# Kernel optimization log

Measured on AMD Instinct MI355X. Metric: run time of the kernel, lower is better.

## Reference

```python
import jax, jax.numpy as jnp
import numpy as np

K = 32
BN_EPS = 1e-5


def _fps(points, n_samples):
    # Sequential farthest point sampling; deterministic start at index 0
    # (torch version uses a random start; math otherwise identical).
    B, N, _ = points.shape

    def step(carry, _):
        dist_min, far = carry                                   # (B,N), (B,)
        c = jnp.take_along_axis(points, far[:, None, None].astype(jnp.int32) * jnp.ones((1, 1, 3), jnp.int32), axis=1)  # (B,1,3)
        d = jnp.sum((points - c) ** 2, axis=2)                  # (B,N)
        dist_min = jnp.minimum(dist_min, d)
        return (dist_min, jnp.argmax(dist_min, axis=1)), far

    init = (jnp.full((B, N), 1e10, points.dtype), jnp.zeros((B,), jnp.int64).astype(jnp.int32))
    _, cent = jax.lax.scan(step, init, None, length=n_samples)  # (n_samples, B)
    return cent.T                                               # (B, n_samples)


def _knn_idx(cntrds, pnts, k):
    # squared euclidean distance (same neighbor ordering as torch.cdist)
    d2 = (jnp.sum(cntrds ** 2, -1)[:, :, None]
          + jnp.sum(pnts ** 2, -1)[:, None, :]
          - 2.0 * jnp.einsum('bsc,bnc->bsn', cntrds, pnts))     # (B,ns,N)
    _, idx = jax.lax.top_k(-d2, k)                              # smallest-k
    return idx                                                  # (B,ns,k)


def _gather(x, idx):
    # x: (B,N,D), idx: (B,...) -> (B,...,D)
    return jax.vmap(lambda a, i: a[i])(x, idx)


def _conv1x1(x, w):
    # x: (B,Cin,ns,k), w: (Cout,Cin)
    return jnp.einsum('oc,bcnk->bonk', w, x)


def _bn_relu(x, g, b):
    # training-mode BatchNorm2d (biased variance over B,ns,k) + ReLU
    mean = jnp.mean(x, axis=(0, 2, 3), keepdims=True)
    var = jnp.var(x, axis=(0, 2, 3), keepdims=True)
    xh = (x - mean) * jax.lax.rsqrt(var + BN_EPS)
    return jax.nn.relu(xh * g[None, :, None, None] + b[None, :, None, None])


def setup_inputs() -> dict:
    key = jax.random.key(0)
    ks = jax.random.split(key, 16)
    B, N = 4, 4096
    s = 0.05
    return {
        'p': jax.random.normal(ks[0], (B, N, 3), jnp.float32),
        'f': jax.random.normal(ks[1], (B, 3, N), jnp.float32),
        'w1': jax.random.normal(ks[2], (256, 6), jnp.float32) * s,
        'w2': jax.random.normal(ks[3], (256, 256), jnp.float32) * s,
        'b2': jax.random.normal(ks[4], (256,), jnp.float32) * s,
        'g2': jnp.ones((256,), jnp.float32),
        'be2': jnp.zeros((256,), jnp.float32),
        'w3': jax.random.normal(ks[5], (512, 512), jnp.float32) * s,
        'g3': jnp.ones((512,), jnp.float32),
        'be3': jnp.zeros((512,), jnp.float32),
        'w4': jax.random.normal(ks[6], (256, 512), jnp.float32) * s,
        'g4': jnp.ones((256,), jnp.float32),
        'be4': jnp.zeros((256,), jnp.float32),
    }


def reference(p, f, w1, w2, b2, g2, be2, w3, g3, be3, w4, g4, be4):
    B, N, _ = p.shape
    ns = N // 4
    idx_c = _fps(p, ns)                                   # (B,ns)
    cntrd = _gather(p, idx_c)                             # (B,ns,3)
    feats = jnp.transpose(f, (0, 2, 1))                   # (B,N,3)
    knn = _knn_idx(cntrd, p, K)                           # (B,ns,K)
    dp = _gather(p, knn)                                  # (B,ns,K,3)
    fj = _gather(feats, knn)                              # (B,ns,K,3)
    x = jnp.transpose(jnp.concatenate([dp, fj], -1), (0, 3, 1, 2))  # (B,6,ns,K)
    # conv1: 6->256 (no bias), 256->256 (bias) + BN + ReLU
    x = _conv1x1(x, w1)
    x = _conv1x1(x, w2) + b2[None, :, None, None]
    x = _bn_relu(x, g2, be2)                              # (B,256,ns,K)
    xm = jnp.max(x, axis=-1, keepdims=True)
    x = jnp.concatenate([jnp.broadcast_to(xm, x.shape), x], axis=1)  # (B,512,ns,K)
    # conv2: 512->512 BN ReLU, 512->256 BN ReLU
    x = _bn_relu(_conv1x1(x, w3), g3, be3)
    x = _bn_relu(_conv1x1(x, w4), g4, be4)
    out_feat = jnp.max(x, axis=-1)                        # (B,256,ns)
    return cntrd, out_feat
```

## Files before the change

### kernel.cpp

```cpp
#include <hip/hip_runtime.h>
#include <hip/hip_bf16.h>

#define B_ 4
#define N_ 4096
#define NS_ 1024
#define KNN_ 32
#define NPOS_ 131072
#define BN_EPS_ 1e-5f

using bf16 = __hip_bfloat16;
typedef unsigned short us;
typedef __attribute__((ext_vector_type(8))) short short8;
typedef __attribute__((ext_vector_type(4))) float f32x4;
typedef unsigned long long ull;

__device__ __forceinline__ float bf2f(bf16 h){ return __bfloat162float(h); }
__device__ __forceinline__ us f2bfbits(float x){
    bf16 h = __float2bfloat16(x);
    return *reinterpret_cast<us*>(&h);
}
__device__ __forceinline__ float bits2f(us u){
    unsigned v = ((unsigned)u)<<16; return __uint_as_float(v);
}
__device__ __forceinline__ void unpack8(uint4 v, float* f){
    f[0]=__uint_as_float((v.x&0xFFFFu)<<16); f[1]=__uint_as_float(v.x&0xFFFF0000u);
    f[2]=__uint_as_float((v.y&0xFFFFu)<<16); f[3]=__uint_as_float(v.y&0xFFFF0000u);
    f[4]=__uint_as_float((v.z&0xFFFFu)<<16); f[5]=__uint_as_float(v.z&0xFFFF0000u);
    f[6]=__uint_as_float((v.w&0xFFFFu)<<16); f[7]=__uint_as_float(v.w&0xFFFF0000u);
}
__device__ __forceinline__ uint4 pack8(const float* f){
    uint4 v;
    v.x = (unsigned)f2bfbits(f[0]) | ((unsigned)f2bfbits(f[1])<<16);
    v.y = (unsigned)f2bfbits(f[2]) | ((unsigned)f2bfbits(f[3])<<16);
    v.z = (unsigned)f2bfbits(f[4]) | ((unsigned)f2bfbits(f[5])<<16);
    v.w = (unsigned)f2bfbits(f[6]) | ((unsigned)f2bfbits(f[7])<<16);
    return v;
}
__device__ __forceinline__ unsigned fmono(float v){
    unsigned u = __float_as_uint(v);
    return (u & 0x80000000u) ? ~u : (u | 0x80000000u);
}

template<int CTRL, int ROWM>
__device__ __forceinline__ float dppmaxf(float x){
    int xi = __float_as_int(x);
    int yi = __builtin_amdgcn_update_dpp(xi, xi, CTRL, ROWM, 0xF, false);
    return fmaxf(x, __int_as_float(yi));
}
template<int CTRL, int ROWM>
__device__ __forceinline__ float dppminf(float x){
    int xi = __float_as_int(x);
    int yi = __builtin_amdgcn_update_dpp(xi, xi, CTRL, ROWM, 0xF, false);
    return fminf(x, __int_as_float(yi));
}
__device__ __forceinline__ float wave_max_f32(float x){
    x = dppmaxf<0x111,0xF>(x);
    x = dppmaxf<0x112,0xF>(x);
    x = dppmaxf<0x114,0xF>(x);
    x = dppmaxf<0x118,0xF>(x);
    x = dppmaxf<0x142,0xA>(x);
    x = dppmaxf<0x143,0xC>(x);
    return __int_as_float(__builtin_amdgcn_readlane(__float_as_int(x), 63));
}
__device__ __forceinline__ float wave_min_f32(float x){
    x = dppminf<0x111,0xF>(x);
    x = dppminf<0x112,0xF>(x);
    x = dppminf<0x114,0xF>(x);
    x = dppminf<0x118,0xF>(x);
    x = dppminf<0x142,0xA>(x);
    x = dppminf<0x143,0xC>(x);
    return __int_as_float(__builtin_amdgcn_readlane(__float_as_int(x), 63));
}
__device__ __forceinline__ float max16(const float* v){
    float a = fmaxf(fmaxf(fmaxf(v[0],v[1]),v[2]),v[3]);
    float b = fmaxf(fmaxf(fmaxf(v[4],v[5]),v[6]),v[7]);
    float c = fmaxf(fmaxf(fmaxf(v[8],v[9]),v[10]),v[11]);
    float d = fmaxf(fmaxf(fmaxf(v[12],v[13]),v[14]),v[15]);
    return fmaxf(fmaxf(a,b), fmaxf(c,d));
}
__device__ __forceinline__ float min16(const float* v){
    float a = fminf(fminf(fminf(v[0],v[1]),v[2]),v[3]);
    float b = fminf(fminf(fminf(v[4],v[5]),v[6]),v[7]);
    float c = fminf(fminf(fminf(v[8],v[9]),v[10]),v[11]);
    float d = fminf(fminf(fminf(v[12],v[13]),v[14]),v[15]);
    return fminf(fminf(a,b), fminf(c,d));
}

__global__ void zero_stats(float* s){ s[blockIdx.x*256 + threadIdx.x] = 0.0f; }

__global__ __launch_bounds__(256) void prep_w26(const float* __restrict__ w1,
                                                const float* __restrict__ w2,
                                                float* __restrict__ W26){
    int c = threadIdx.x;
    float acc[6] = {0,0,0,0,0,0};
    for (int k=0;k<256;k++){
        float w2v = w2[c*256+k];
        #pragma unroll
        for (int j=0;j<6;j++) acc[j] = fmaf(w2v, w1[k*6+j], acc[j]);
    }
    #pragma unroll
    for (int j=0;j<6;j++) W26[j*256+c] = acc[j];
}

__global__ __launch_bounds__(256) void prep_whl(const float* __restrict__ w, int n,
                                                us* __restrict__ hi,
                                                us* __restrict__ lo){
    int i = blockIdx.x*256 + threadIdx.x;
    if (i < n){
        float x = w[i];
        us h = f2bfbits(x);
        hi[i] = h;
        lo[i] = f2bfbits(__fsub_rn(x, bits2f(h)));
    }
}

__global__ __launch_bounds__(256) void bn_coef(const float* __restrict__ sums,
                                               const float* __restrict__ g,
                                               const float* __restrict__ be,
                                               int C, float2* __restrict__ ab){
    int c = blockIdx.x*256 + threadIdx.x;
    if (c < C){
        const float inv = 1.0f/(float)NPOS_;
        float mean = sums[c*2+0]*inv;
        float var  = sums[c*2+1]*inv - mean*mean;
        float a = g[c]*rsqrtf(var + BN_EPS_);
        ab[c] = make_float2(a, be[c] - mean*a);
    }
}

__global__ __launch_bounds__(256) void fps_kernel(const float* __restrict__ p,
                                                  int* __restrict__ idxc,
                                                  float* __restrict__ cntrd){
    __shared__ float4 pxyz[N_];
    __shared__ ull warr[2][4];
    const int b = blockIdx.x;
    const int t = threadIdx.x;
    const int lane = t & 63;
    const int wave = t >> 6;
    const float* pb = p + (size_t)b*N_*3;
    float rx[16], ry[16], rz[16], dist[16];
    #pragma unroll
    for (int j=0;j<16;j++){
        int i = t*16+j;
        float x = pb[i*3+0];
        float y = pb[i*3+1];
        float z = pb[i*3+2];
        rx[j]=x; ry[j]=y; rz[j]=z;
        pxyz[i] = make_float4(x,y,z,0.f);
        dist[j]=1e10f;
    }
    __syncthreads();
    int cur = 0;
    float4 c = pxyz[0];
    if (t==0){
        idxc[b*NS_] = 0;
        cntrd[(size_t)(b*NS_)*3+0] = c.x;
        cntrd[(size_t)(b*NS_)*3+1] = c.y;
        cntrd[(size_t)(b*NS_)*3+2] = c.z;
    }
    for (int s=1; s<NS_; s++){
        #pragma unroll
        for (int j=0;j<16;j++){
            float dx = __fsub_rn(rx[j],c.x);
            float dy = __fsub_rn(ry[j],c.y);
            float dz = __fsub_rn(rz[j],c.z);
            float d  = __fadd_rn(__fadd_rn(__fmul_rn(dx,dx),__fmul_rn(dy,dy)),__fmul_rn(dz,dz));
            dist[j] = fminf(dist[j], d);
        }
        float lmax = max16(dist);
        float wmax = wave_max_f32(lmax);
        unsigned msk = 0;
        #pragma unroll
        for (int j=0;j<16;j++) msk |= (dist[j]==wmax) ? (1u<<j) : 0u;
        ull ball = __ballot(msk != 0);
        int srclane = (int)__builtin_ctzll(ball);
        unsigned lmsk = (unsigned)__builtin_amdgcn_readlane((int)msk, srclane);
        int widx = (wave*64 + srclane)*16 + (int)__builtin_ctz(lmsk);
        if (lane==0)
            warr[s&1][wave] = ((ull)__float_as_uint(wmax)<<32) | (0xFFFFFFFFu - (unsigned)widx);
        __syncthreads();
        ull g0 = warr[s&1][0], g1 = warr[s&1][1], g2 = warr[s&1][2], g3 = warr[s&1][3];
        ull ga = g0 > g1 ? g0 : g1;
        ull gb = g2 > g3 ? g2 : g3;
        ull g  = ga > gb ? ga : gb;
        cur = (int)(0xFFFFFFFFu - (unsigned)(g & 0xFFFFFFFFull));
        c = pxyz[cur];
        if (t==0){
            idxc[b*NS_+s] = cur;
            cntrd[(size_t)(b*NS_+s)*3+0] = c.x;
            cntrd[(size_t)(b*NS_+s)*3+1] = c.y;
            cntrd[(size_t)(b*NS_+s)*3+2] = c.z;
        }
    }
}

__global__ __launch_bounds__(256) void knn_kernel(const float* __restrict__ p,
                                                  const int* __restrict__ idxc,
                                                  int* __restrict__ knn){
    __shared__ ull warr[2][4];
    const int bid = blockIdx.x;
    const int b = bid >> 10;
    const int t = threadIdx.x;
    const int lane = t & 63;
    const int wave = t >> 6;
    const float* pb = p + (size_t)b*N_*3;
    const int ci = idxc[bid];
    float cx = pb[ci*3+0];
    float cy = pb[ci*3+1];
    float cz = pb[ci*3+2];
    float c2 = __fadd_rn(__fadd_rn(__fmul_rn(cx,cx),__fmul_rn(cy,cy)),__fmul_rn(cz,cz));
    float d2[16];
    #pragma unroll
    for (int j=0;j<16;j++){
        int i = t*16+j;
        float x = pb[i*3+0];
        float y = pb[i*3+1];
        float z = pb[i*3+2];
        float p2 = __fadd_rn(__fadd_rn(__fmul_rn(x,x),__fmul_rn(y,y)),__fmul_rn(z,z));
        float dot= __fadd_rn(__fadd_rn(__fmul_rn(cx,x),__fmul_rn(cy,y)),__fmul_rn(cz,z));
        d2[j] = __fsub_rn(__fadd_rn(c2,p2), __fmul_rn(2.0f,dot));
    }
    for (int it=0; it<KNN_; it++){
        float lmin = min16(d2);
        float wmin = wave_min_f32(lmin);
        unsigned msk = 0;
        #pragma unroll
        for (int j=0;j<16;j++) msk |= (d2[j]==wmin) ? (1u<<j) : 0u;
        ull ball = __ballot(msk != 0);
        int srclane = (int)__builtin_ctzll(ball);
        unsigned lmsk = (unsigned)__builtin_amdgcn_readlane((int)msk, srclane);
        int widx = (wave*64 + srclane)*16 + (int)__builtin_ctz(lmsk);
        if (lane==0)
            warr[it&1][wave] = ((ull)fmono(wmin)<<32) | (unsigned)widx;
        __syncthreads();
        ull g0 = warr[it&1][0], g1 = warr[it&1][1], g2 = warr[it&1][2], g3 = warr[it&1][3];
        ull ga = g0 < g1 ? g0 : g1;
        ull gb = g2 < g3 ? g2 : g3;
        ull g  = ga < gb ? ga : gb;
        int idx = (int)(g & 0xFFFFFFFFull);
        if ((idx>>4)==t) d2[idx & 15] = INFINITY;
        if (t==0) knn[(size_t)bid*KNN_ + it] = idx;
    }
}

__global__ __launch_bounds__(256) void conv12_kernel(const float* __restrict__ p,
                                                     const float* __restrict__ f,
                                                     const int* __restrict__ knn,
                                                     const float* __restrict__ W26,
                                                     const float* __restrict__ b2,
                                                     bf16* __restrict__ z2){
    __shared__ float Ws[6][256];
    __shared__ float xs[6][32];
    const int bid = blockIdx.x;
    const int b = bid >> 10;
    const int t = threadIdx.x;
    #pragma unroll
    for (int r=0;r<6;r++) Ws[r][t] = W26[r*256+t];
    if (t < 32){
        int i = knn[(size_t)bid*KNN_ + t];
        const float* pb = p + (size_t)b*N_*3;
        const float* fb = f + (size_t)b*3*N_;
        xs[0][t] = pb[i*3+0];
        xs[1][t] = pb[i*3+1];
        xs[2][t] = pb[i*3+2];
        xs[3][t] = fb[0*N_+i];
        xs[4][t] = fb[1*N_+i];
        xs[5][t] = fb[2*N_+i];
    }
    __syncthreads();
    float w0=Ws[0][t], w1v=Ws[1][t], w2v=Ws[2][t], w3v=Ws[3][t], w4v=Ws[4][t], w5v=Ws[5][t];
    float bias = b2[t];
    bf16* zrow = z2 + (size_t)t*NPOS_ + (size_t)bid*KNN_;
    for (int k0=0;k0<32;k0+=8){
        float y[8];
        #pragma unroll
        for (int u=0;u<8;u++){
            int k = k0+u;
            float acc = bias;
            acc = fmaf(w0, xs[0][k], acc);
            acc = fmaf(w1v,xs[1][k], acc);
            acc = fmaf(w2v,xs[2][k], acc);
            acc = fmaf(w3v,xs[3][k], acc);
            acc = fmaf(w4v,xs[4][k], acc);
            acc = fmaf(w5v,xs[5][k], acc);
            y[u] = acc;
        }
        *reinterpret_cast<uint4*>(zrow + k0) = pack8(y);
    }
}

__global__ __launch_bounds__(256) void stats_kernel(const bf16* __restrict__ z,
                                                    float* __restrict__ sums){
    __shared__ float sw[4], qw[4];
    const int c = blockIdx.y;
    const int chunk = blockIdx.x;
    const int t = threadIdx.x;
    const bf16* zp = z + (size_t)c*NPOS_ + (size_t)chunk*16384;
    const uint4* zp4 = reinterpret_cast<const uint4*>(zp);
    float s=0.f, q=0.f;
    for (int r=0;r<8;r++){
        uint4 v = zp4[r*256 + t];
        float fv[8]; unpack8(v, fv);
        #pragma unroll
        for (int u=0;u<8;u++){ s += fv[u]; q = fmaf(fv[u], fv[u], q); }
    }
    #pragma unroll
    for (int m=1;m<64;m<<=1){ s += __shfl_xor(s,m,64); q += __shfl_xor(q,m,64); }
    if ((t&63)==0){ sw[t>>6]=s; qw[t>>6]=q; }
    __syncthreads();
    if (t==0){
        s = sw[0]+sw[1]+sw[2]+sw[3];
        q = qw[0]+qw[1]+qw[2]+qw[3];
        atomicAdd(&sums[c*2+0], s);
        atomicAdd(&sums[c*2+1], q);
    }
}

__global__ __launch_bounds__(256) void xm_kernel(const bf16* __restrict__ z2raw,
                                                 const float2* __restrict__ ab,
                                                 bf16* __restrict__ xm){
    int gid = blockIdx.x*256 + threadIdx.x;
    int c = gid >> 12;
    int bs = gid & 4095;
    float2 s = ab[c];
    const uint4* xp = reinterpret_cast<const uint4*>(z2raw + (size_t)c*NPOS_ + (size_t)bs*KNN_);
    float m = 0.0f;
    #pragma unroll
    for (int r=0;r<4;r++){
        uint4 v = xp[r];
        float fv[8]; unpack8(v, fv);
        #pragma unroll
        for (int u=0;u<8;u++) m = fmaxf(m, fmaf(fv[u], s.x, s.y));
    }
    xm[(size_t)c*4096 + bs] = __float2bfloat16(m);
}

__global__ __launch_bounds__(256) void gemm128(const float* __restrict__ A, int lda, int aoff,
                                               const bf16* __restrict__ B,
                                               int M, int N, int K,
                                               float* __restrict__ Cf){
    __shared__ float As[16][128];
    __shared__ float Bs[16][128];
    const int tid = threadIdx.x;
    const int tx = tid & 15, ty = tid >> 4;
    const int m0 = blockIdx.y*128, n0 = blockIdx.x*128;
    float acc[8][8];
    #pragma unroll
    for (int i=0;i<8;i++)
        #pragma unroll
        for (int j=0;j<8;j++) acc[i][j]=0.f;
    const int arow = tid >> 1, akg = tid & 1;
    const int bkk = tid >> 4, bng = tid & 15;
    for (int k0=0;k0<K;k0+=16){
        const float* aptr = A + (size_t)(m0+arow)*lda + aoff + k0 + akg*8;
        float4 a0 = *reinterpret_cast<const float4*>(aptr);
        float4 a1 = *reinterpret_cast<const float4*>(aptr+4);
        As[akg*8+0][arow]=a0.x; As[akg*8+1][arow]=a0.y;
        As[akg*8+2][arow]=a0.z; As[akg*8+3][arow]=a0.w;
        As[akg*8+4][arow]=a1.x; As[akg*8+5][arow]=a1.y;
        As[akg*8+6][arow]=a1.z; As[akg*8+7][arow]=a1.w;
        uint4 bv = *reinterpret_cast<const uint4*>(B + (size_t)(k0+bkk)*N + n0 + bng*8);
        float bf[8]; unpack8(bv, bf);
        *reinterpret_cast<float4*>(&Bs[bkk][bng*8+0]) = make_float4(bf[0],bf[1],bf[2],bf[3]);
        *reinterpret_cast<float4*>(&Bs[bkk][bng*8+4]) = make_float4(bf[4],bf[5],bf[6],bf[7]);
        __syncthreads();
        #pragma unroll
        for (int kk=0;kk<16;kk++){
            float a[8], b[8];
            *reinterpret_cast<float4*>(&a[0]) = *reinterpret_cast<float4*>(&As[kk][ty*8+0]);
            *reinterpret_cast<float4*>(&a[4]) = *reinterpret_cast<float4*>(&As[kk][ty*8+4]);
            *reinterpret_cast<float4*>(&b[0]) = *reinterpret_cast<float4*>(&Bs[kk][tx*8+0]);
            *reinterpret_cast<float4*>(&b[4]) = *reinterpret_cast<float4*>(&Bs[kk][tx*8+4]);
            #pragma unroll
            for (int i=0;i<8;i++)
                #pragma unroll
                for (int j=0;j<8;j++)
                    acc[i][j] = fmaf(a[i], b[j], acc[i][j]);
        }
        __syncthreads();
    }
    const int n = n0 + tx*8;
    #pragma unroll
    for (int i=0;i<8;i++){
        int m = m0 + ty*8 + i;
        *reinterpret_cast<float4*>(Cf + (size_t)m*N + n + 0) = make_float4(acc[i][0],acc[i][1],acc[i][2],acc[i][3]);
        *reinterpret_cast<float4*>(Cf + (size_t)m*N + n + 4) = make_float4(acc[i][4],acc[i][5],acc[i][6],acc[i][7]);
    }
}

#define LDK 40
__global__ __launch_bounds__(256) void gemm_mfma(const us* __restrict__ Whi,
                                                 const us* __restrict__ Wlo,
                                                 int ldw, int aoff,
                                                 const bf16* __restrict__ act, int K,
                                                 const float2* __restrict__ ab,
                                                 bf16* __restrict__ out,
                                                 const float* __restrict__ t3){
    __shared__ __align__(16) us AsH[128*LDK];
    __shared__ __align__(16) us AsL[128*LDK];
    __shared__ __align__(16) us Bs [128*LDK];
    __shared__ float t3s[128][4];
    const us* actu = reinterpret_cast<const us*>(act);
    const int t = threadIdx.x;
    const int m0 = blockIdx.x*128, n0 = blockIdx.y*128;
    const int wave = t>>6, lane = t&63;
    const int wm = wave>>1, wn = wave&1;
    const int q = lane>>4, col = lane&15;

    if (t3 && t < 128){
        const float* src = t3 + (size_t)(m0+t)*4096 + (n0>>5);
        t3s[t][0]=src[0]; t3s[t][1]=src[1]; t3s[t][2]=src[2]; t3s[t][3]=src[3];
    }

    f32x4 acc[4][4];
    #pragma unroll
    for (int i=0;i<4;i++)
        #pragma unroll
        for (int j=0;j<4;j++) acc[i][j] = (f32x4){0.f,0.f,0.f,0.f};

    const int ar = t>>1, ah = t&1;
    const int bn = t&127, bh = t>>7;

    for (int k0=0;k0<K;k0+=32){
        const us* sh = Whi + (size_t)(m0+ar)*ldw + aoff + k0 + ah*16;
        const us* sl = Wlo + (size_t)(m0+ar)*ldw + aoff + k0 + ah*16;
        uint4 h0 = *reinterpret_cast<const uint4*>(sh);
        uint4 h1 = *reinterpret_cast<const uint4*>(sh+8);
        uint4 l0 = *reinterpret_cast<const uint4*>(sl);
        uint4 l1 = *reinterpret_cast<const uint4*>(sl+8);
        *reinterpret_cast<uint4*>(&AsH[ar*LDK + ah*16 + 0]) = h0;
        *reinterpret_cast<uint4*>(&AsH[ar*LDK + ah*16 + 8]) = h1;
        *reinterpret_cast<uint4*>(&AsL[ar*LDK + ah*16 + 0]) = l0;
        *reinterpret_cast<uint4*>(&AsL[ar*LDK + ah*16 + 8]) = l1;
        us bvals[16];
        #pragma unroll
        for (int j=0;j<16;j++){
            int k = k0 + bh*16 + j;
            float x = bits2f(actu[(size_t)k*NPOS_ + n0 + bn]);
            float2 s = ab[k];
            bvals[j] = f2bfbits(fmaxf(fmaf(x, s.x, s.y), 0.0f));
        }
        *reinterpret_cast<uint4*>(&Bs[bn*LDK + bh*16 + 0]) = *reinterpret_cast<uint4*>(&bvals[0]);
        *reinterpret_cast<uint4*>(&Bs[bn*LDK + bh*16 + 8]) = *reinterpret_cast<uint4*>(&bvals[8]);
        __syncthreads();
        short8 bf[4], afh[4], afl[4];
        #pragma unroll
        for (int tn=0;tn<4;tn++)
            bf[tn] = *reinterpret_cast<const short8*>(&Bs[(wn*64+tn*16+col)*LDK + q*8]);
        #pragma unroll
        for (int tm=0;tm<4;tm++){
            afh[tm] = *reinterpret_cast<const short8*>(&AsH[(wm*64+tm*16+col)*LDK + q*8]);
            afl[tm] = *reinterpret_cast<const short8*>(&AsL[(wm*64+tm*16+col)*LDK + q*8]);
        }
        #pragma unroll
        for (int tm=0;tm<4;tm++)
            #pragma unroll
            for (int tn=0;tn<4;tn++){
                acc[tm][tn] = __builtin_amdgcn_mfma_f32_16x16x32_bf16(afh[tm], bf[tn], acc[tm][tn], 0, 0, 0);
                acc[tm][tn] = __builtin_amdgcn_mfma_f32_16x16x32_bf16(afl[tm], bf[tn], acc[tm][tn], 0, 0, 0);
            }
        __syncthreads();
    }
    #pragma unroll
    for (int tm=0;tm<4;tm++){
        #pragma unroll
        for (int tn=0;tn<4;tn++){
            int n_l = wn*64 + tn*16 + col;
            #pragma unroll
            for (int r=0;r<4;r++){
                int m_l = wm*64 + tm*16 + q*4 + r;
                float vv = acc[tm][tn][r];
                if (t3) vv += t3s[m_l][n_l>>5];
                out[(size_t)(m0+m_l)*NPOS_ + n0 + n_l] = __float2bfloat16(vv);
            }
        }
    }
}

__global__ __launch_bounds__(256) void final_kernel(const bf16* __restrict__ z4,
                                                    const float* __restrict__ sums,
                                                    const float* __restrict__ g,
                                                    const float* __restrict__ be,
                                                    float* __restrict__ out){
    int gid = blockIdx.x*256 + threadIdx.x;
    int s = gid & 1023;
    int c = (gid >> 10) & 255;
    int b = gid >> 18;
    int bsi = b*NS_ + s;
    const float inv = 1.0f/(float)NPOS_;
    float mean = sums[c*2+0]*inv;
    float var  = sums[c*2+1]*inv - mean*mean;
    float rs = rsqrtf(var + BN_EPS_);
    float a  = g[c]*rs;
    float bb = be[c] - mean*a;
    const uint4* zp = reinterpret_cast<const uint4*>(z4 + (size_t)c*NPOS_ + (size_t)bsi*KNN_);
    float m = -INFINITY;
    #pragma unroll
    for (int r=0;r<4;r++){
        uint4 v = zp[r];
        float fv[8]; unpack8(v, fv);
        #pragma unroll
        for (int u=0;u<8;u++) m = fmaxf(m, fmaf(fv[u], a, bb));
    }
    m = fmaxf(m, 0.0f);
    out[(size_t)(b*256 + c)*NS_ + s] = m;
}

extern "C" void kernel_launch(void* const* d_in, const int* in_sizes, int n_in,
                              void* d_out, int out_size, void* d_ws, size_t ws_size,
                              hipStream_t stream) {
    const float* p   = (const float*)d_in[0];
    const float* f   = (const float*)d_in[1];
    const float* w1  = (const float*)d_in[2];
    const float* w2  = (const float*)d_in[3];
    const float* b2  = (const float*)d_in[4];
    const float* g2  = (const float*)d_in[5];
    const float* be2 = (const float*)d_in[6];
    const float* w3  = (const float*)d_in[7];
    const float* g3  = (const float*)d_in[8];
    const float* be3 = (const float*)d_in[9];
    const float* w4  = (const float*)d_in[10];
    const float* g4  = (const float*)d_in[11];
    const float* be4 = (const float*)d_in[12];

    char* ws = (char*)d_ws;
    int*    idxc = (int*)(ws + 0);
    int*    knn  = (int*)(ws + 16384);
    float*  W26  = (float*)(ws + 540672);
    float*  stats= (float*)(ws + 546816);
    float2* ab2  = (float2*)(ws + 555008);
    float2* ab3  = (float2*)(ws + 557056);
    us* whi3 = (us*)(ws + 561152);
    us* wlo3 = (us*)(ws + 1085440);
    us* whi4 = (us*)(ws + 1609728);
    us* wlo4 = (us*)(ws + 1871872);
    float*  t3   = (float*)(ws + 2134016);
    bf16*   z2   = (bf16*)(ws + 10522624);
    bf16*   xm   = (bf16*)(ws + 77631488);
    bf16*   z3   = (bf16*)(ws + 79728640);
    bf16*   z4   = z2;

    float* out_cntrd = (float*)d_out;
    float* out_feat  = (float*)d_out + (size_t)B_*NS_*3;

    zero_stats<<<8, 256, 0, stream>>>(stats);
    prep_w26<<<1, 256, 0, stream>>>(w1, w2, W26);
    prep_whl<<<1024, 256, 0, stream>>>(w3, 512*512, whi3, wlo3);
    prep_whl<<<512, 256, 0, stream>>>(w4, 256*512, whi4, wlo4);
    fps_kernel<<<B_, 256, 0, stream>>>(p, idxc, out_cntrd);
    knn_kernel<<<B_*NS_, 256, 0, stream>>>(p, idxc, knn);
    conv12_kernel<<<B_*NS_, 256, 0, stream>>>(p, f, knn, W26, b2, z2);
    stats_kernel<<<dim3(8,256), 256, 0, stream>>>(z2, stats);
    bn_coef<<<1, 256, 0, stream>>>(stats, g2, be2, 256, ab2);
    xm_kernel<<<4096, 256, 0, stream>>>(z2, ab2, xm);
    gemm128<<<dim3(32,4), 256, 0, stream>>>(w3, 512, 0, xm, 512, 4096, 256, t3);
    gemm_mfma<<<dim3(4,1024), 256, 0, stream>>>(whi3, wlo3, 512, 256, z2, 256, ab2, z3, t3);
    stats_kernel<<<dim3(8,512), 256, 0, stream>>>(z3, stats + 512);
    bn_coef<<<2, 256, 0, stream>>>(stats + 512, g3, be3, 512, ab3);
    gemm_mfma<<<dim3(2,1024), 256, 0, stream>>>(whi4, wlo4, 512, 0, z3, 512, ab3, z4, nullptr);
    stats_kernel<<<dim3(8,256), 256, 0, stream>>>(z4, stats + 1536);
    final_kernel<<<4096, 256, 0, stream>>>(z4, stats + 1536, g4, be4, out_feat);
}
```

Before: 1.242 ms.

## Fuse BN statistics into producers, merge knn with conv12, fold prep into fps

Folds the weight-prep and stats-zeroing kernels into extra blocks of the FPS launch so they run alongside the four FPS blocks. Merges the kNN selection with the first conv so the neighbour indices stay in shared memory, and computes the BN sum and sum-of-squares inside the conv and MFMA GEMM epilogues with DPP row reductions and atomics. This removes three full re-reads of the large bf16 activation tensors and several launches. In exchange it adds many atomics per channel and extra epilogue work, and the order of the float summation changes.

```diff
diff --git a/kernel.cpp b/kernel.cpp
--- a/kernel.cpp
+++ b/kernel.cpp
@@ -71,6 +71,13 @@
     x = dppminf<0x143,0xC>(x);
     return __int_as_float(__builtin_amdgcn_readlane(__float_as_int(x), 63));
 }
+__device__ __forceinline__ float rowsum16(float x){
+    x += __int_as_float(__builtin_amdgcn_update_dpp(0, __float_as_int(x), 0x111, 0xF, 0xF, true));
+    x += __int_as_float(__builtin_amdgcn_update_dpp(0, __float_as_int(x), 0x112, 0xF, 0xF, true));
+    x += __int_as_float(__builtin_amdgcn_update_dpp(0, __float_as_int(x), 0x114, 0xF, 0xF, true));
+    x += __int_as_float(__builtin_amdgcn_update_dpp(0, __float_as_int(x), 0x118, 0xF, 0xF, true));
+    return x;
+}
 __device__ __forceinline__ float max16(const float* v){
     float a = fmaxf(fmaxf(fmaxf(v[0],v[1]),v[2]),v[3]);
     float b = fmaxf(fmaxf(fmaxf(v[4],v[5]),v[6]),v[7]);
@@ -84,34 +91,6 @@
     float c = fminf(fminf(fminf(v[8],v[9]),v[10]),v[11]);
     float d = fminf(fminf(fminf(v[12],v[13]),v[14]),v[15]);
     return fminf(fminf(a,b), fminf(c,d));
-}
-
-__global__ void zero_stats(float* s){ s[blockIdx.x*256 + threadIdx.x] = 0.0f; }
-
-__global__ __launch_bounds__(256) void prep_w26(const float* __restrict__ w1,
-                                                const float* __restrict__ w2,
-                                                float* __restrict__ W26){
-    int c = threadIdx.x;
-    float acc[6] = {0,0,0,0,0,0};
-    for (int k=0;k<256;k++){
-        float w2v = w2[c*256+k];
-        #pragma unroll
-        for (int j=0;j<6;j++) acc[j] = fmaf(w2v, w1[k*6+j], acc[j]);
-    }
-    #pragma unroll
-    for (int j=0;j<6;j++) W26[j*256+c] = acc[j];
-}
-
-__global__ __launch_bounds__(256) void prep_whl(const float* __restrict__ w, int n,
-                                                us* __restrict__ hi,
-                                                us* __restrict__ lo){
-    int i = blockIdx.x*256 + threadIdx.x;
-    if (i < n){
-        float x = w[i];
-        us h = f2bfbits(x);
-        hi[i] = h;
-        lo[i] = f2bfbits(__fsub_rn(x, bits2f(h)));
-    }
 }
 
 __global__ __launch_bounds__(256) void bn_coef(const float* __restrict__ sums,
@@ -128,13 +107,49 @@
     }
 }
 
-__global__ __launch_bounds__(256) void fps_kernel(const float* __restrict__ p,
-                                                  int* __restrict__ idxc,
-                                                  float* __restrict__ cntrd){
+__global__ __launch_bounds__(256) void fps_plus(const float* __restrict__ p,
+                                                int* __restrict__ idxc,
+                                                float* __restrict__ cntrd,
+                                                float* __restrict__ stats,
+                                                const float* __restrict__ w1,
+                                                const float* __restrict__ w2,
+                                                float* __restrict__ W26,
+                                                const float* __restrict__ w3,
+                                                us* __restrict__ whi3, us* __restrict__ wlo3,
+                                                const float* __restrict__ w4,
+                                                us* __restrict__ whi4, us* __restrict__ wlo4){
     __shared__ float4 pxyz[N_];
     __shared__ ull warr[2][4];
-    const int b = blockIdx.x;
+    const int bid = blockIdx.x;
     const int t = threadIdx.x;
+    if (bid >= 4){
+        if (bid < 12){
+            stats[(bid-4)*256 + t] = 0.0f;
+        } else if (bid == 12){
+            float acc[6] = {0,0,0,0,0,0};
+            for (int k=0;k<256;k++){
+                float w2v = w2[t*256+k];
+                #pragma unroll
+                for (int j=0;j<6;j++) acc[j] = fmaf(w2v, w1[k*6+j], acc[j]);
+            }
+            #pragma unroll
+            for (int j=0;j<6;j++) W26[j*256+t] = acc[j];
+        } else if (bid < 1037){
+            int i = (bid-13)*256 + t;
+            float x = w3[i];
+            us h = f2bfbits(x);
+            whi3[i] = h;
+            wlo3[i] = f2bfbits(__fsub_rn(x, bits2f(h)));
+        } else {
+            int i = (bid-1037)*256 + t;
+            float x = w4[i];
+            us h = f2bfbits(x);
+            whi4[i] = h;
+            wlo4[i] = f2bfbits(__fsub_rn(x, bits2f(h)));
+        }
+        return;
+    }
+    const int b = bid;
     const int lane = t & 63;
     const int wave = t >> 6;
     const float* pb = p + (size_t)b*N_*3;
@@ -194,16 +209,25 @@
     }
 }
 
-__global__ __launch_bounds__(256) void knn_kernel(const float* __restrict__ p,
-                                                  const int* __restrict__ idxc,
-                                                  int* __restrict__ knn){
+__global__ __launch_bounds__(256) void convknn_kernel(const float* __restrict__ p,
+                                                      const float* __restrict__ f,
+                                                      const int* __restrict__ idxc,
+                                                      const float* __restrict__ W26,
+                                                      const float* __restrict__ b2,
+                                                      bf16* __restrict__ z2,
+                                                      float* __restrict__ sums){
     __shared__ ull warr[2][4];
+    __shared__ int knnS[32];
+    __shared__ float Ws[6][256];
+    __shared__ float xs[6][32];
     const int bid = blockIdx.x;
     const int b = bid >> 10;
     const int t = threadIdx.x;
     const int lane = t & 63;
     const int wave = t >> 6;
     const float* pb = p + (size_t)b*N_*3;
+    #pragma unroll
+    for (int r=0;r<6;r++) Ws[r][t] = W26[r*256+t];
     const int ci = idxc[bid];
     float cx = pb[ci*3+0];
     float cy = pb[ci*3+1];
@@ -239,26 +263,11 @@
         ull g  = ga < gb ? ga : gb;
         int idx = (int)(g & 0xFFFFFFFFull);
         if ((idx>>4)==t) d2[idx & 15] = INFINITY;
-        if (t==0) knn[(size_t)bid*KNN_ + it] = idx;
-    }
-}
-
-__global__ __launch_bounds__(256) void conv12_kernel(const float* __restrict__ p,
-                                                     const float* __restrict__ f,
-                                                     const int* __restrict__ knn,
-                                                     const float* __restrict__ W26,
-                                                     const float* __restrict__ b2,
-                                                     bf16* __restrict__ z2){
-    __shared__ float Ws[6][256];
-    __shared__ float xs[6][32];
-    const int bid = blockIdx.x;
-    const int b = bid >> 10;
-    const int t = threadIdx.x;
-    #pragma unroll
-    for (int r=0;r<6;r++) Ws[r][t] = W26[r*256+t];
+        if (t==0) knnS[it] = idx;
+    }
+    __syncthreads();
     if (t < 32){
-        int i = knn[(size_t)bid*KNN_ + t];
-        const float* pb = p + (size_t)b*N_*3;
+        int i = knnS[t];
         const float* fb = f + (size_t)b*3*N_;
         xs[0][t] = pb[i*3+0];
         xs[1][t] = pb[i*3+1];
@@ -271,6 +280,7 @@
     float w0=Ws[0][t], w1v=Ws[1][t], w2v=Ws[2][t], w3v=Ws[3][t], w4v=Ws[4][t], w5v=Ws[5][t];
     float bias = b2[t];
     bf16* zrow = z2 + (size_t)t*NPOS_ + (size_t)bid*KNN_;
+    float ssum = 0.f, sq = 0.f;
     for (int k0=0;k0<32;k0+=8){
         float y[8];
         #pragma unroll
@@ -283,37 +293,14 @@
             acc = fmaf(w3v,xs[3][k], acc);
             acc = fmaf(w4v,xs[4][k], acc);
             acc = fmaf(w5v,xs[5][k], acc);
+            float vr = bits2f(f2bfbits(acc));
+            ssum += vr; sq = fmaf(vr, vr, sq);
             y[u] = acc;
         }
         *reinterpret_cast<uint4*>(zrow + k0) = pack8(y);
     }
-}
-
-__global__ __launch_bounds__(256) void stats_kernel(const bf16* __restrict__ z,
-                                                    float* __restrict__ sums){
-    __shared__ float sw[4], qw[4];
-    const int c = blockIdx.y;
-    const int chunk = blockIdx.x;
-    const int t = threadIdx.x;
-    const bf16* zp = z + (size_t)c*NPOS_ + (size_t)chunk*16384;
-    const uint4* zp4 = reinterpret_cast<const uint4*>(zp);
-    float s=0.f, q=0.f;
-    for (int r=0;r<8;r++){
-        uint4 v = zp4[r*256 + t];
-        float fv[8]; unpack8(v, fv);
-        #pragma unroll
-        for (int u=0;u<8;u++){ s += fv[u]; q = fmaf(fv[u], fv[u], q); }
-    }
-    #pragma unroll
-    for (int m=1;m<64;m<<=1){ s += __shfl_xor(s,m,64); q += __shfl_xor(q,m,64); }
-    if ((t&63)==0){ sw[t>>6]=s; qw[t>>6]=q; }
-    __syncthreads();
-    if (t==0){
-        s = sw[0]+sw[1]+sw[2]+sw[3];
-        q = qw[0]+qw[1]+qw[2]+qw[3];
-        atomicAdd(&sums[c*2+0], s);
-        atomicAdd(&sums[c*2+1], q);
-    }
+    atomicAdd(&sums[t*2+0], ssum);
+    atomicAdd(&sums[t*2+1], sq);
 }
 
 __global__ __launch_bounds__(256) void xm_kernel(const bf16* __restrict__ z2raw,
@@ -395,7 +382,8 @@
                                                  const bf16* __restrict__ act, int K,
                                                  const float2* __restrict__ ab,
                                                  bf16* __restrict__ out,
-                                                 const float* __restrict__ t3){
+                                                 const float* __restrict__ t3,
+                                                 float* __restrict__ sums){
     __shared__ __align__(16) us AsH[128*LDK];
     __shared__ __align__(16) us AsL[128*LDK];
     __shared__ __align__(16) us Bs [128*LDK];
@@ -464,14 +452,24 @@
     #pragma unroll
     for (int tm=0;tm<4;tm++){
         #pragma unroll
-        for (int tn=0;tn<4;tn++){
-            int n_l = wn*64 + tn*16 + col;
+        for (int r=0;r<4;r++){
+            int m_l = wm*64 + tm*16 + q*4 + r;
+            float srow = 0.f, qrow = 0.f;
             #pragma unroll
-            for (int r=0;r<4;r++){
-                int m_l = wm*64 + tm*16 + q*4 + r;
+            for (int tn=0;tn<4;tn++){
+                int n_l = wn*64 + tn*16 + col;
                 float vv = acc[tm][tn][r];
                 if (t3) vv += t3s[m_l][n_l>>5];
-                out[(size_t)(m0+m_l)*NPOS_ + n0 + n_l] = __float2bfloat16(vv);
+                us hb = f2bfbits(vv);
+                reinterpret_cast<us*>(out)[(size_t)(m0+m_l)*NPOS_ + n0 + n_l] = hb;
+                float vr = bits2f(hb);
+                srow += vr; qrow = fmaf(vr, vr, qrow);
+            }
+            srow = rowsum16(srow);
+            qrow = rowsum16(qrow);
+            if (col == 15){
+                atomicAdd(&sums[(m0+m_l)*2+0], srow);
+                atomicAdd(&sums[(m0+m_l)*2+1], qrow);
             }
         }
     }
@@ -525,7 +523,6 @@
 
     char* ws = (char*)d_ws;
     int*    idxc = (int*)(ws + 0);
-    int*    knn  = (int*)(ws + 16384);
     float*  W26  = (float*)(ws + 540672);
     float*  stats= (float*)(ws + 546816);
     float2* ab2  = (float2*)(ws + 555008);
@@ -543,21 +540,14 @@
     float* out_cntrd = (float*)d_out;
     float* out_feat  = (float*)d_out + (size_t)B_*NS_*3;
 
-    zero_stats<<<8, 256, 0, stream>>>(stats);
-    prep_w26<<<1, 256, 0, stream>>>(w1, w2, W26);
-    prep_whl<<<1024, 256, 0, stream>>>(w3, 512*512, whi3, wlo3);
-    prep_whl<<<512, 256, 0, stream>>>(w4, 256*512, whi4, wlo4);
-    fps_kernel<<<B_, 256, 0, stream>>>(p, idxc, out_cntrd);
-    knn_kernel<<<B_*NS_, 256, 0, stream>>>(p, idxc, knn);
-    conv12_kernel<<<B_*NS_, 256, 0, stream>>>(p, f, knn, W26, b2, z2);
-    stats_kernel<<<dim3(8,256), 256, 0, stream>>>(z2, stats);
+    fps_plus<<<1549, 256, 0, stream>>>(p, idxc, out_cntrd, stats,
+                                       w1, w2, W26, w3, whi3, wlo3, w4, whi4, wlo4);
+    convknn_kernel<<<B_*NS_, 256, 0, stream>>>(p, f, idxc, W26, b2, z2, stats);
     bn_coef<<<1, 256, 0, stream>>>(stats, g2, be2, 256, ab2);
     xm_kernel<<<4096, 256, 0, stream>>>(z2, ab2, xm);
     gemm128<<<dim3(32,4), 256, 0, stream>>>(w3, 512, 0, xm, 512, 4096, 256, t3);
-    gemm_mfma<<<dim3(4,1024), 256, 0, stream>>>(whi3, wlo3, 512, 256, z2, 256, ab2, z3, t3);
-    stats_kernel<<<dim3(8,512), 256, 0, stream>>>(z3, stats + 512);
+    gemm_mfma<<<dim3(4,1024), 256, 0, stream>>>(whi3, wlo3, 512, 256, z2, 256, ab2, z3, t3, stats + 512);
     bn_coef<<<2, 256, 0, stream>>>(stats + 512, g3, be3, 512, ab3);
-    gemm_mfma<<<dim3(2,1024), 256, 0, stream>>>(whi4, wlo4, 512, 0, z3, 512, ab3, z4, nullptr);
-    stats_kernel<<<dim3(8,256), 256, 0, stream>>>(z4, stats + 1536);
+    gemm_mfma<<<dim3(2,1024), 256, 0, stream>>>(whi4, wlo4, 512, 0, z3, 512, ab3, z4, nullptr, stats + 1536);
     final_kernel<<<4096, 256, 0, stream>>>(z4, stats + 1536, g4, be4, out_feat);
 }
```

Measured after the change: 2.011 ms. 61.8% more time.
